# Kernel optimization log

Hardware: AMD Instinct MI355X
Metric: run time of the kernel (lower is better)

The kernel has to match this reference:

```python
import jax, jax.numpy as jnp
import numpy as np

B, S, D = 4, 2048, 512
H = 8
DEPTH = D // H  # 64


def setup_inputs() -> dict:
    key = jax.random.key(0)
    ks = jax.random.split(key, 6)
    scale = 1.0 / np.sqrt(D)
    return {
        "x": jax.random.normal(ks[0], (B, S, D), dtype=jnp.float32),
        "y": jax.random.normal(ks[1], (B, S, D), dtype=jnp.float32),
        "W_q": jax.random.normal(ks[2], (D, D), dtype=jnp.float32) * scale,
        "W_k": jax.random.normal(ks[3], (D, D), dtype=jnp.float32) * scale,
        "W_v": jax.random.normal(ks[4], (D, D), dtype=jnp.float32) * scale,
        "W_o": jax.random.normal(ks[5], (D, D), dtype=jnp.float32) * scale,
    }


def _split_heads(t):
    # [B, S, D] -> [B, H, S, DEPTH]
    b, s, _ = t.shape
    return t.reshape(b, s, H, DEPTH).transpose(0, 2, 1, 3)


def reference(x, y, W_q, W_k, W_v, W_o):
    q = _split_heads(x @ W_q) * (DEPTH ** -0.5)   # [B,H,Sq,d]
    k = _split_heads(y @ W_k)                      # [B,H,Sk,d]
    v = _split_heads(y @ W_v)                      # [B,H,Sk,d]
    logits = jnp.einsum("bhqd,bhkd->bhqk", q, k)   # [B,H,Sq,Sk]
    weights = jax.nn.softmax(logits, axis=-1)
    attn = jnp.einsum("bhqk,bhkd->bhqd", weights, v)  # [B,H,Sq,d]
    attn = attn.transpose(0, 2, 1, 3).reshape(x.shape[0], x.shape[1], D)
    return attn @ W_o
```

## Files before the change

kernel.cpp:

```cpp
#include <hip/hip_runtime.h>
#include <hip/hip_bf16.h>
#include <math.h>
#include <stdint.h>

#define NB 4
#define NS 2048
#define ND 512
#define NH 8
#define DEP 64

typedef __attribute__((ext_vector_type(8))) short bf16x8;
typedef __attribute__((ext_vector_type(4))) short bf16x4;
typedef __attribute__((ext_vector_type(4))) float f32x4;

#define QSCALE 0.18033688011112042f

__device__ __forceinline__ short f2b(float f) {
  unsigned u = __float_as_uint(f);
  u += 0x7FFF + ((u >> 16) & 1);
  return (short)(u >> 16);
}
__device__ __forceinline__ unsigned pk2(float a, float b) {
  union { __hip_bfloat162 h; unsigned u; } c;
  c.h = __float22bfloat162_rn(float2{a, b});
  return c.u;
}
__device__ __forceinline__ void dma16(const void* g, void* l) {
  __builtin_amdgcn_global_load_lds(
      (const __attribute__((address_space(1))) void*)g,
      (__attribute__((address_space(3))) void*)l, 16, 0, 0);
}

__global__ __launch_bounds__(256) void prep(
    const float* __restrict__ x, const float* __restrict__ y,
    const float* __restrict__ W0, const float* __restrict__ W1,
    const float* __restrict__ W2, const float* __restrict__ W3,
    short* __restrict__ xb, short* __restrict__ yb, short* __restrict__ T0,
    short* __restrict__ T1, short* __restrict__ T2, short* __restrict__ T3) {
  const int t = threadIdx.x;
  if (blockIdx.y < 2) {
    const float* src = blockIdx.y ? y : x;
    short* dst = blockIdx.y ? yb : xb;
    size_t i = ((size_t)blockIdx.x * 256 + t) * 4;
    float4 v = *(const float4*)(src + i);
    bf16x4 o;
    o[0] = f2b(v.x); o[1] = f2b(v.y); o[2] = f2b(v.z); o[3] = f2b(v.w);
    *(bf16x4*)(dst + i) = o;
    return;
  }
  const int bx = blockIdx.x;
  if (bx >= 256) return;
  const int wj = bx >> 6, rem = bx & 63;
  const float* W = wj == 0 ? W0 : wj == 1 ? W1 : wj == 2 ? W2 : W3;
  short* T = wj == 0 ? T0 : wj == 1 ? T1 : wj == 2 ? T2 : T3;
  __shared__ float tile[64][65];
  const int k0 = (rem >> 3) * 64, n0 = (rem & 7) * 64;
#pragma unroll
  for (int i = 0; i < 4; ++i) {
    int r = (t >> 4) + i * 16;
    int c = (t & 15) * 4;
    float4 v = *(const float4*)&W[(size_t)(k0 + r) * ND + n0 + c];
    tile[r][c] = v.x; tile[r][c + 1] = v.y;
    tile[r][c + 2] = v.z; tile[r][c + 3] = v.w;
  }
  __syncthreads();
#pragma unroll
  for (int i = 0; i < 4; ++i) {
    int n = (t >> 4) + i * 16;
    int kc = (t & 15) * 4;
    bf16x4 o;
#pragma unroll
    for (int j = 0; j < 4; ++j) o[j] = f2b(tile[kc + j][n]);
    *(bf16x4*)&T[(size_t)(n0 + n) * ND + k0 + kc] = o;
  }
}

__device__ __forceinline__ void gemm128(const short* __restrict__ A,
                                        const short* __restrict__ Bt,
                                        short* __restrict__ Cout, int mode,
                                        float alpha) {
  __shared__ short As[128 * 64];
  __shared__ short Bs[128 * 64];
  const int t = threadIdx.x;
  const int wave = t >> 6, lane = t & 63;
  const int m = lane & 15, quad = lane >> 4;
  const int m0 = blockIdx.y * 128, n0 = blockIdx.x * 128;
  const int mh = (wave >> 1) * 64, nh = (wave & 1) * 64;
  const int r8 = lane >> 3;
  const int c8 = (lane & 7) ^ r8;
  const int mx7 = m & 7;
  f32x4 acc[4][4];
#pragma unroll
  for (int i = 0; i < 4; ++i)
#pragma unroll
    for (int j = 0; j < 4; ++j) acc[i][j] = (f32x4){0.f, 0.f, 0.f, 0.f};

  for (int k0 = 0; k0 < ND; k0 += 64) {
    __syncthreads();
#pragma unroll
    for (int i = 0; i < 4; ++i) {
      int row = i * 32 + wave * 8 + r8;
      dma16(A + (size_t)(m0 + row) * ND + k0 + c8 * 8,
            As + (i * 256 + wave * 64) * 8);
      dma16(Bt + (size_t)(n0 + row) * ND + k0 + c8 * 8,
            Bs + (i * 256 + wave * 64) * 8);
    }
    __syncthreads();
    bf16x8 af[4][2], bf[4][2];
#pragma unroll
    for (int mt = 0; mt < 4; ++mt)
#pragma unroll
      for (int kc = 0; kc < 2; ++kc)
        af[mt][kc] = *(const bf16x8*)(As + (mh + mt * 16 + m) * 64 +
                                      ((kc * 4 + quad) ^ mx7) * 8);
#pragma unroll
    for (int nt = 0; nt < 4; ++nt)
#pragma unroll
      for (int kc = 0; kc < 2; ++kc)
        bf[nt][kc] = *(const bf16x8*)(Bs + (nh + nt * 16 + m) * 64 +
                                      ((kc * 4 + quad) ^ mx7) * 8);
#pragma unroll
    for (int mt = 0; mt < 4; ++mt)
#pragma unroll
      for (int nt = 0; nt < 4; ++nt)
#pragma unroll
        for (int kc = 0; kc < 2; ++kc)
          acc[mt][nt] = __builtin_amdgcn_mfma_f32_16x16x32_bf16(
              af[mt][kc], bf[nt][kc], acc[mt][nt], 0, 0, 0);
  }
  if (mode == 2) {
#pragma unroll
    for (int mt = 0; mt < 4; ++mt)
#pragma unroll
      for (int nt = 0; nt < 4; ++nt) {
        int row0 = m0 + mh + mt * 16 + quad * 4;
        int col = n0 + nh + nt * 16 + m;
        int b_ = row0 >> 11, s_ = row0 & (NS - 1);
        int h_ = col >> 6, d_ = col & (DEP - 1);
        uint2 p;
        p.x = pk2(acc[mt][nt][0] * alpha, acc[mt][nt][1] * alpha);
        p.y = pk2(acc[mt][nt][2] * alpha, acc[mt][nt][3] * alpha);
        *(uint2*)(Cout + (size_t)((b_ * NH + h_) * DEP + d_) * NS + s_) = p;
      }
  } else {
#pragma unroll
    for (int mt = 0; mt < 4; ++mt)
#pragma unroll
      for (int nt = 0; nt < 4; ++nt)
#pragma unroll
        for (int r = 0; r < 4; ++r) {
          int row = m0 + mh + mt * 16 + quad * 4 + r;
          int col = n0 + nh + nt * 16 + m;
          Cout[(size_t)row * ND + col] = f2b(acc[mt][nt][r] * alpha);
        }
  }
}

__global__ __launch_bounds__(256) void qkv_gemm(
    const short* __restrict__ xb, const short* __restrict__ yb,
    const short* __restrict__ Wqt, const short* __restrict__ Wkt,
    const short* __restrict__ Wvt, short* __restrict__ Qb,
    short* __restrict__ Kb, short* __restrict__ Vtb) {
  if (blockIdx.z == 0)
    gemm128(xb, Wqt, Qb, 1, QSCALE);
  else if (blockIdx.z == 1)
    gemm128(yb, Wkt, Kb, 1, 1.0f);
  else
    gemm128(yb, Wvt, Vtb, 2, 1.0f);
}

__global__ __launch_bounds__(256) void out_gemm(const short* __restrict__ A,
                                                const short* __restrict__ Bt,
                                                float* __restrict__ Cout) {
  __shared__ short As[2][128 * 64];
  __shared__ short Bs[2][64 * 64];
  const int t = threadIdx.x;
  const int wave = t >> 6, lane = t & 63;
  const int m = lane & 15, quad = lane >> 4;
  const int m0 = blockIdx.y * 128, n0 = blockIdx.x * 64;
  const int mh = (wave >> 1) * 64, nh = (wave & 1) * 32;
  const int r8 = lane >> 3;
  const int c8 = (lane & 7) ^ r8;
  const int mx7 = m & 7;
  f32x4 acc[4][2];
#pragma unroll
  for (int i = 0; i < 4; ++i)
#pragma unroll
    for (int j = 0; j < 2; ++j) acc[i][j] = (f32x4){0.f, 0.f, 0.f, 0.f};

#pragma unroll
  for (int i = 0; i < 4; ++i)
    dma16(A + (size_t)(m0 + i * 32 + wave * 8 + r8) * ND + c8 * 8,
          As[0] + (i * 256 + wave * 64) * 8);
#pragma unroll
  for (int i = 0; i < 2; ++i)
    dma16(Bt + (size_t)(n0 + i * 32 + wave * 8 + r8) * ND + c8 * 8,
          Bs[0] + (i * 256 + wave * 64) * 8);

  int buf = 0;
  for (int k0 = 0; k0 < ND; k0 += 64, buf ^= 1) {
    __syncthreads();
    if (k0 + 64 < ND) {
#pragma unroll
      for (int i = 0; i < 4; ++i)
        dma16(A + (size_t)(m0 + i * 32 + wave * 8 + r8) * ND + k0 + 64 + c8 * 8,
              As[buf ^ 1] + (i * 256 + wave * 64) * 8);
#pragma unroll
      for (int i = 0; i < 2; ++i)
        dma16(Bt + (size_t)(n0 + i * 32 + wave * 8 + r8) * ND + k0 + 64 +
                  c8 * 8,
              Bs[buf ^ 1] + (i * 256 + wave * 64) * 8);
    }
    bf16x8 af[4][2], bf[2][2];
#pragma unroll
    for (int mt = 0; mt < 4; ++mt)
#pragma unroll
      for (int kc = 0; kc < 2; ++kc)
        af[mt][kc] = *(const bf16x8*)(As[buf] + (mh + mt * 16 + m) * 64 +
                                      ((kc * 4 + quad) ^ mx7) * 8);
#pragma unroll
    for (int nt = 0; nt < 2; ++nt)
#pragma unroll
      for (int kc = 0; kc < 2; ++kc)
        bf[nt][kc] = *(const bf16x8*)(Bs[buf] + (nh + nt * 16 + m) * 64 +
                                      ((kc * 4 + quad) ^ mx7) * 8);
#pragma unroll
    for (int mt = 0; mt < 4; ++mt)
#pragma unroll
      for (int nt = 0; nt < 2; ++nt)
#pragma unroll
        for (int kc = 0; kc < 2; ++kc)
          acc[mt][nt] = __builtin_amdgcn_mfma_f32_16x16x32_bf16(
              af[mt][kc], bf[nt][kc], acc[mt][nt], 0, 0, 0);
  }
#pragma unroll
  for (int mt = 0; mt < 4; ++mt)
#pragma unroll
    for (int nt = 0; nt < 2; ++nt)
#pragma unroll
      for (int r = 0; r < 4; ++r) {
        int row = m0 + mh + mt * 16 + quad * 4 + r;
        int col = n0 + nh + nt * 16 + m;
        Cout[(size_t)row * ND + col] = acc[mt][nt][r];
      }
}

__global__ __launch_bounds__(256) void attn_mfma(const short* __restrict__ Qb,
                                                 const short* __restrict__ Kb,
                                                 const short* __restrict__ Vtb,
                                                 short* __restrict__ Ob) {
  __shared__ short Ks[2][64 * 64];
  __shared__ short Vts[2][64 * 64];
  __shared__ short Pt[64 * 64];
  const int t = threadIdx.x;
  const int wave = t >> 6, lane = t & 63;
  const int m = lane & 15, quad = lane >> 4;
  const int bh = blockIdx.y, b = bh >> 3, h = bh & 7;
  const int q0 = blockIdx.x * 64;
  const int wq = wave * 16;
  const size_t rowb = (size_t)b * NS;
  const short* Vtbase = Vtb + (size_t)(bh * DEP) * NS;
  const int r8 = lane >> 3;
  const int c8 = (lane & 7) ^ r8;
  const int mx7 = m & 7;

  bf16x8 qf[2];
#pragma unroll
  for (int kc = 0; kc < 2; ++kc)
    qf[kc] = *(const bf16x8*)(Qb + (rowb + q0 + wq + m) * ND + h * DEP +
                              kc * 32 + quad * 8);

  float l_ = 0.0f;
  f32x4 Ot[4];
#pragma unroll
  for (int mt = 0; mt < 4; ++mt) Ot[mt] = (f32x4){0.f, 0.f, 0.f, 0.f};

#pragma unroll
  for (int i = 0; i < 2; ++i) {
    int row = i * 32 + wave * 8 + r8;
    dma16(Kb + (rowb + row) * ND + h * DEP + c8 * 8,
          Ks[0] + (i * 256 + wave * 64) * 8);
    dma16(Vtbase + (size_t)row * NS + c8 * 8,
          Vts[0] + (i * 256 + wave * 64) * 8);
  }

  int buf = 0;
  for (int kv0 = 0; kv0 < NS; kv0 += 64, buf ^= 1) {
    __syncthreads();
    if (kv0 + 64 < NS) {
#pragma unroll
      for (int i = 0; i < 2; ++i) {
        int row = i * 32 + wave * 8 + r8;
        dma16(Kb + (rowb + kv0 + 64 + row) * ND + h * DEP + c8 * 8,
              Ks[buf ^ 1] + (i * 256 + wave * 64) * 8);
        dma16(Vtbase + (size_t)row * NS + kv0 + 64 + c8 * 8,
              Vts[buf ^ 1] + (i * 256 + wave * 64) * 8);
      }
    }

    f32x4 St[4];
#pragma unroll
    for (int mt = 0; mt < 4; ++mt) St[mt] = (f32x4){0.f, 0.f, 0.f, 0.f};
#pragma unroll
    for (int mt = 0; mt < 4; ++mt)
#pragma unroll
      for (int kc = 0; kc < 2; ++kc) {
        bf16x8 kf = *(const bf16x8*)(Ks[buf] + (mt * 16 + m) * 64 +
                                     ((kc * 4 + quad) ^ mx7) * 8);
        St[mt] = __builtin_amdgcn_mfma_f32_16x16x32_bf16(kf, qf[kc], St[mt],
                                                         0, 0, 0);
      }

    float rs = 0.0f;
#pragma unroll
    for (int mt = 0; mt < 4; ++mt) {
      float p0 = __builtin_amdgcn_exp2f(St[mt][0]);
      float p1 = __builtin_amdgcn_exp2f(St[mt][1]);
      float p2 = __builtin_amdgcn_exp2f(St[mt][2]);
      float p3 = __builtin_amdgcn_exp2f(St[mt][3]);
      rs += (p0 + p1) + (p2 + p3);
      uint2 pk;
      pk.x = pk2(p0, p1);
      pk.y = pk2(p2, p3);
      *(uint2*)(Pt + (wq + m) * 64 + ((mt * 2 + (quad >> 1)) ^ mx7) * 8 +
                (quad & 1) * 4) = pk;
    }
    l_ += rs;

#pragma unroll
    for (int kc = 0; kc < 2; ++kc) {
      bf16x8 pf = *(const bf16x8*)(Pt + (wq + m) * 64 +
                                   ((kc * 4 + quad) ^ mx7) * 8);
#pragma unroll
      for (int mt = 0; mt < 4; ++mt) {
        bf16x8 vf = *(const bf16x8*)(Vts[buf] + (mt * 16 + m) * 64 +
                                     ((kc * 4 + quad) ^ mx7) * 8);
        Ot[mt] = __builtin_amdgcn_mfma_f32_16x16x32_bf16(vf, pf, Ot[mt],
                                                         0, 0, 0);
      }
    }
  }

  l_ += __shfl_xor(l_, 16, 64);
  l_ += __shfl_xor(l_, 32, 64);
  float linv = 1.0f / l_;
  size_t row = rowb + q0 + wq + m;
#pragma unroll
  for (int mt = 0; mt < 4; ++mt)
#pragma unroll
    for (int r = 0; r < 4; ++r)
      Ob[row * ND + h * DEP + mt * 16 + quad * 4 + r] = f2b(Ot[mt][r] * linv);
}

extern "C" void kernel_launch(void* const* d_in, const int* in_sizes, int n_in,
                              void* d_out, int out_size, void* d_ws,
                              size_t ws_size, hipStream_t stream) {
  const float* x = (const float*)d_in[0];
  const float* y = (const float*)d_in[1];
  const float* Wq = (const float*)d_in[2];
  const float* Wk = (const float*)d_in[3];
  const float* Wv = (const float*)d_in[4];
  const float* Wo = (const float*)d_in[5];
  float* out = (float*)d_out;

  const size_t mat = (size_t)NB * NS * ND;
  const size_t wsz = (size_t)ND * ND;
  short* xb = (short*)d_ws;
  short* yb = xb + mat;
  short* Wqt = yb + mat;
  short* Wkt = Wqt + wsz;
  short* Wvt = Wkt + wsz;
  short* Wot = Wvt + wsz;
  short* Qb = Wot + wsz;
  short* Kb = Qb + mat;
  short* Vtb = Kb + mat;
  short* attnb = xb;

  prep<<<dim3(mat / 1024, 3), 256, 0, stream>>>(x, y, Wq, Wk, Wv, Wo, xb, yb,
                                                Wqt, Wkt, Wvt, Wot);
  qkv_gemm<<<dim3(ND / 128, (NB * NS) / 128, 3), 256, 0, stream>>>(
      xb, yb, Wqt, Wkt, Wvt, Qb, Kb, Vtb);
  attn_mfma<<<dim3(NS / 64, NB * NH), 256, 0, stream>>>(Qb, Kb, Vtb, attnb);
  out_gemm<<<dim3(ND / 64, (NB * NS) / 128), 256, 0, stream>>>(attnb, Wot,
                                                               out);
}
```

Baseline: 186.4 us.

## Fuse K/V projections sharing y tiles and split attention KV across waves

The QKV GEMM now uses 128x64 tiles. The z=1 blocks compute both K and V from one shared y tile, so y is loaded once for both projections, though Q and KV blocks now carry uneven work. The attention kernel changes its wave split: each wave handles 32 queries against half of each 64-key tile instead of 16 queries against the whole tile. Partial outputs and row sums are then combined through shared memory at the end, which adds an epilogue sync and reduction in exchange for better reuse of K fragments.

```diff
diff --git a/kernel.cpp b/kernel.cpp
--- a/kernel.cpp
+++ b/kernel.cpp
@@ -75,38 +75,52 @@
   }
 }
 
-__device__ __forceinline__ void gemm128(const short* __restrict__ A,
-                                        const short* __restrict__ Bt,
-                                        short* __restrict__ Cout, int mode,
-                                        float alpha) {
+__global__ __launch_bounds__(256) void qkv_gemm(
+    const short* __restrict__ xb, const short* __restrict__ yb,
+    const short* __restrict__ Wqt, const short* __restrict__ Wkt,
+    const short* __restrict__ Wvt, short* __restrict__ Qb,
+    short* __restrict__ Kb, short* __restrict__ Vtb) {
   __shared__ short As[128 * 64];
-  __shared__ short Bs[128 * 64];
+  __shared__ short B0s[64 * 64];
+  __shared__ short B1s[64 * 64];
+  const int z = blockIdx.z;
+  const short* A = z ? yb : xb;
+  const short* Bt0 = z ? Wkt : Wqt;
   const int t = threadIdx.x;
   const int wave = t >> 6, lane = t & 63;
   const int m = lane & 15, quad = lane >> 4;
-  const int m0 = blockIdx.y * 128, n0 = blockIdx.x * 128;
-  const int mh = (wave >> 1) * 64, nh = (wave & 1) * 64;
+  const int m0 = blockIdx.y * 128, n0 = blockIdx.x * 64;
+  const int mh = (wave >> 1) * 64, nh = (wave & 1) * 32;
   const int r8 = lane >> 3;
   const int c8 = (lane & 7) ^ r8;
   const int mx7 = m & 7;
-  f32x4 acc[4][4];
+  f32x4 acc0[4][2], acc1[4][2];
 #pragma unroll
   for (int i = 0; i < 4; ++i)
 #pragma unroll
-    for (int j = 0; j < 4; ++j) acc[i][j] = (f32x4){0.f, 0.f, 0.f, 0.f};
+    for (int j = 0; j < 2; ++j) {
+      acc0[i][j] = (f32x4){0.f, 0.f, 0.f, 0.f};
+      acc1[i][j] = (f32x4){0.f, 0.f, 0.f, 0.f};
+    }
 
   for (int k0 = 0; k0 < ND; k0 += 64) {
     __syncthreads();
 #pragma unroll
-    for (int i = 0; i < 4; ++i) {
-      int row = i * 32 + wave * 8 + r8;
-      dma16(A + (size_t)(m0 + row) * ND + k0 + c8 * 8,
+    for (int i = 0; i < 4; ++i)
+      dma16(A + (size_t)(m0 + i * 32 + wave * 8 + r8) * ND + k0 + c8 * 8,
             As + (i * 256 + wave * 64) * 8);
-      dma16(Bt + (size_t)(n0 + row) * ND + k0 + c8 * 8,
-            Bs + (i * 256 + wave * 64) * 8);
+#pragma unroll
+    for (int i = 0; i < 2; ++i)
+      dma16(Bt0 + (size_t)(n0 + i * 32 + wave * 8 + r8) * ND + k0 + c8 * 8,
+            B0s + (i * 256 + wave * 64) * 8);
+    if (z) {
+#pragma unroll
+      for (int i = 0; i < 2; ++i)
+        dma16(Wvt + (size_t)(n0 + i * 32 + wave * 8 + r8) * ND + k0 + c8 * 8,
+              B1s + (i * 256 + wave * 64) * 8);
     }
     __syncthreads();
-    bf16x8 af[4][2], bf[4][2];
+    bf16x8 af[4][2], bf0[2][2];
 #pragma unroll
     for (int mt = 0; mt < 4; ++mt)
 #pragma unroll
@@ -114,59 +128,64 @@
         af[mt][kc] = *(const bf16x8*)(As + (mh + mt * 16 + m) * 64 +
                                       ((kc * 4 + quad) ^ mx7) * 8);
 #pragma unroll
-    for (int nt = 0; nt < 4; ++nt)
+    for (int nt = 0; nt < 2; ++nt)
 #pragma unroll
       for (int kc = 0; kc < 2; ++kc)
-        bf[nt][kc] = *(const bf16x8*)(Bs + (nh + nt * 16 + m) * 64 +
-                                      ((kc * 4 + quad) ^ mx7) * 8);
-#pragma unroll
-    for (int mt = 0; mt < 4; ++mt)
-#pragma unroll
-      for (int nt = 0; nt < 4; ++nt)
+        bf0[nt][kc] = *(const bf16x8*)(B0s + (nh + nt * 16 + m) * 64 +
+                                       ((kc * 4 + quad) ^ mx7) * 8);
+#pragma unroll
+    for (int mt = 0; mt < 4; ++mt)
+#pragma unroll
+      for (int nt = 0; nt < 2; ++nt)
 #pragma unroll
         for (int kc = 0; kc < 2; ++kc)
-          acc[mt][nt] = __builtin_amdgcn_mfma_f32_16x16x32_bf16(
-              af[mt][kc], bf[nt][kc], acc[mt][nt], 0, 0, 0);
-  }
-  if (mode == 2) {
-#pragma unroll
-    for (int mt = 0; mt < 4; ++mt)
-#pragma unroll
-      for (int nt = 0; nt < 4; ++nt) {
+          acc0[mt][nt] = __builtin_amdgcn_mfma_f32_16x16x32_bf16(
+              af[mt][kc], bf0[nt][kc], acc0[mt][nt], 0, 0, 0);
+    if (z) {
+      bf16x8 bf1[2][2];
+#pragma unroll
+      for (int nt = 0; nt < 2; ++nt)
+#pragma unroll
+        for (int kc = 0; kc < 2; ++kc)
+          bf1[nt][kc] = *(const bf16x8*)(B1s + (nh + nt * 16 + m) * 64 +
+                                         ((kc * 4 + quad) ^ mx7) * 8);
+#pragma unroll
+      for (int mt = 0; mt < 4; ++mt)
+#pragma unroll
+        for (int nt = 0; nt < 2; ++nt)
+#pragma unroll
+          for (int kc = 0; kc < 2; ++kc)
+            acc1[mt][nt] = __builtin_amdgcn_mfma_f32_16x16x32_bf16(
+                af[mt][kc], bf1[nt][kc], acc1[mt][nt], 0, 0, 0);
+    }
+  }
+  short* C0 = z ? Kb : Qb;
+  const float alpha0 = z ? 1.0f : QSCALE;
+#pragma unroll
+  for (int mt = 0; mt < 4; ++mt)
+#pragma unroll
+    for (int nt = 0; nt < 2; ++nt)
+#pragma unroll
+      for (int r = 0; r < 4; ++r) {
+        int row = m0 + mh + mt * 16 + quad * 4 + r;
+        int col = n0 + nh + nt * 16 + m;
+        C0[(size_t)row * ND + col] = f2b(acc0[mt][nt][r] * alpha0);
+      }
+  if (z) {
+#pragma unroll
+    for (int mt = 0; mt < 4; ++mt)
+#pragma unroll
+      for (int nt = 0; nt < 2; ++nt) {
         int row0 = m0 + mh + mt * 16 + quad * 4;
         int col = n0 + nh + nt * 16 + m;
         int b_ = row0 >> 11, s_ = row0 & (NS - 1);
         int h_ = col >> 6, d_ = col & (DEP - 1);
         uint2 p;
-        p.x = pk2(acc[mt][nt][0] * alpha, acc[mt][nt][1] * alpha);
-        p.y = pk2(acc[mt][nt][2] * alpha, acc[mt][nt][3] * alpha);
-        *(uint2*)(Cout + (size_t)((b_ * NH + h_) * DEP + d_) * NS + s_) = p;
-      }
-  } else {
-#pragma unroll
-    for (int mt = 0; mt < 4; ++mt)
-#pragma unroll
-      for (int nt = 0; nt < 4; ++nt)
-#pragma unroll
-        for (int r = 0; r < 4; ++r) {
-          int row = m0 + mh + mt * 16 + quad * 4 + r;
-          int col = n0 + nh + nt * 16 + m;
-          Cout[(size_t)row * ND + col] = f2b(acc[mt][nt][r] * alpha);
-        }
-  }
-}
-
-__global__ __launch_bounds__(256) void qkv_gemm(
-    const short* __restrict__ xb, const short* __restrict__ yb,
-    const short* __restrict__ Wqt, const short* __restrict__ Wkt,
-    const short* __restrict__ Wvt, short* __restrict__ Qb,
-    short* __restrict__ Kb, short* __restrict__ Vtb) {
-  if (blockIdx.z == 0)
-    gemm128(xb, Wqt, Qb, 1, QSCALE);
-  else if (blockIdx.z == 1)
-    gemm128(yb, Wkt, Kb, 1, 1.0f);
-  else
-    gemm128(yb, Wvt, Vtb, 2, 1.0f);
+        p.x = pk2(acc1[mt][nt][0], acc1[mt][nt][1]);
+        p.y = pk2(acc1[mt][nt][2], acc1[mt][nt][3]);
+        *(uint2*)(Vtb + (size_t)((b_ * NH + h_) * DEP + d_) * NS + s_) = p;
+      }
+  }
 }
 
 __global__ __launch_bounds__(256) void out_gemm(const short* __restrict__ A,
@@ -255,25 +274,30 @@
   const int t = threadIdx.x;
   const int wave = t >> 6, lane = t & 63;
   const int m = lane & 15, quad = lane >> 4;
+  const int kh = wave >> 1, qh = wave & 1;
   const int bh = blockIdx.y, b = bh >> 3, h = bh & 7;
   const int q0 = blockIdx.x * 64;
-  const int wq = wave * 16;
   const size_t rowb = (size_t)b * NS;
   const short* Vtbase = Vtb + (size_t)(bh * DEP) * NS;
   const int r8 = lane >> 3;
   const int c8 = (lane & 7) ^ r8;
   const int mx7 = m & 7;
 
-  bf16x8 qf[2];
-#pragma unroll
-  for (int kc = 0; kc < 2; ++kc)
-    qf[kc] = *(const bf16x8*)(Qb + (rowb + q0 + wq + m) * ND + h * DEP +
-                              kc * 32 + quad * 8);
-
-  float l_ = 0.0f;
-  f32x4 Ot[4];
-#pragma unroll
-  for (int mt = 0; mt < 4; ++mt) Ot[mt] = (f32x4){0.f, 0.f, 0.f, 0.f};
+  bf16x8 qf[2][2];
+#pragma unroll
+  for (int nt = 0; nt < 2; ++nt)
+#pragma unroll
+    for (int kc = 0; kc < 2; ++kc)
+      qf[nt][kc] =
+          *(const bf16x8*)(Qb + (rowb + q0 + qh * 32 + nt * 16 + m) * ND +
+                           h * DEP + kc * 32 + quad * 8);
+
+  float l_[2] = {0.0f, 0.0f};
+  f32x4 Ot[4][2];
+#pragma unroll
+  for (int mt = 0; mt < 4; ++mt)
+#pragma unroll
+    for (int nt = 0; nt < 2; ++nt) Ot[mt][nt] = (f32x4){0.f, 0.f, 0.f, 0.f};
 
 #pragma unroll
   for (int i = 0; i < 2; ++i) {
@@ -298,58 +322,101 @@
       }
     }
 
-    f32x4 St[4];
-#pragma unroll
-    for (int mt = 0; mt < 4; ++mt) St[mt] = (f32x4){0.f, 0.f, 0.f, 0.f};
-#pragma unroll
-    for (int mt = 0; mt < 4; ++mt)
+    f32x4 St[2][2];
+#pragma unroll
+    for (int mt = 0; mt < 2; ++mt)
+#pragma unroll
+      for (int nt = 0; nt < 2; ++nt) St[mt][nt] = (f32x4){0.f, 0.f, 0.f, 0.f};
+#pragma unroll
+    for (int mt = 0; mt < 2; ++mt)
 #pragma unroll
       for (int kc = 0; kc < 2; ++kc) {
-        bf16x8 kf = *(const bf16x8*)(Ks[buf] + (mt * 16 + m) * 64 +
-                                     ((kc * 4 + quad) ^ mx7) * 8);
-        St[mt] = __builtin_amdgcn_mfma_f32_16x16x32_bf16(kf, qf[kc], St[mt],
-                                                         0, 0, 0);
-      }
-
-    float rs = 0.0f;
-#pragma unroll
-    for (int mt = 0; mt < 4; ++mt) {
-      float p0 = __builtin_amdgcn_exp2f(St[mt][0]);
-      float p1 = __builtin_amdgcn_exp2f(St[mt][1]);
-      float p2 = __builtin_amdgcn_exp2f(St[mt][2]);
-      float p3 = __builtin_amdgcn_exp2f(St[mt][3]);
-      rs += (p0 + p1) + (p2 + p3);
-      uint2 pk;
-      pk.x = pk2(p0, p1);
-      pk.y = pk2(p2, p3);
-      *(uint2*)(Pt + (wq + m) * 64 + ((mt * 2 + (quad >> 1)) ^ mx7) * 8 +
-                (quad & 1) * 4) = pk;
-    }
-    l_ += rs;
-
-#pragma unroll
-    for (int kc = 0; kc < 2; ++kc) {
-      bf16x8 pf = *(const bf16x8*)(Pt + (wq + m) * 64 +
-                                   ((kc * 4 + quad) ^ mx7) * 8);
+        bf16x8 kf =
+            *(const bf16x8*)(Ks[buf] + (kh * 32 + mt * 16 + m) * 64 +
+                             ((kc * 4 + quad) ^ mx7) * 8);
+#pragma unroll
+        for (int nt = 0; nt < 2; ++nt)
+          St[mt][nt] = __builtin_amdgcn_mfma_f32_16x16x32_bf16(
+              kf, qf[nt][kc], St[mt][nt], 0, 0, 0);
+      }
+
+#pragma unroll
+    for (int nt = 0; nt < 2; ++nt) {
+      float rs = 0.0f;
+#pragma unroll
+      for (int mt = 0; mt < 2; ++mt) {
+        float p0 = __builtin_amdgcn_exp2f(St[mt][nt][0]);
+        float p1 = __builtin_amdgcn_exp2f(St[mt][nt][1]);
+        float p2 = __builtin_amdgcn_exp2f(St[mt][nt][2]);
+        float p3 = __builtin_amdgcn_exp2f(St[mt][nt][3]);
+        rs += (p0 + p1) + (p2 + p3);
+        uint2 pk;
+        pk.x = pk2(p0, p1);
+        pk.y = pk2(p2, p3);
+        *(uint2*)(Pt + (qh * 32 + nt * 16 + m) * 64 +
+                  ((kh * 4 + mt * 2 + (quad >> 1)) ^ mx7) * 8 +
+                  (quad & 1) * 4) = pk;
+      }
+      l_[nt] += rs;
+    }
+
+#pragma unroll
+    for (int nt = 0; nt < 2; ++nt) {
+      bf16x8 pf = *(const bf16x8*)(Pt + (qh * 32 + nt * 16 + m) * 64 +
+                                   ((kh * 4 + quad) ^ mx7) * 8);
 #pragma unroll
       for (int mt = 0; mt < 4; ++mt) {
         bf16x8 vf = *(const bf16x8*)(Vts[buf] + (mt * 16 + m) * 64 +
-                                     ((kc * 4 + quad) ^ mx7) * 8);
-        Ot[mt] = __builtin_amdgcn_mfma_f32_16x16x32_bf16(vf, pf, Ot[mt],
-                                                         0, 0, 0);
-      }
-    }
-  }
-
-  l_ += __shfl_xor(l_, 16, 64);
-  l_ += __shfl_xor(l_, 32, 64);
-  float linv = 1.0f / l_;
-  size_t row = rowb + q0 + wq + m;
-#pragma unroll
-  for (int mt = 0; mt < 4; ++mt)
-#pragma unroll
-    for (int r = 0; r < 4; ++r)
-      Ob[row * ND + h * DEP + mt * 16 + quad * 4 + r] = f2b(Ot[mt][r] * linv);
+                                     ((kh * 4 + quad) ^ mx7) * 8);
+        Ot[mt][nt] = __builtin_amdgcn_mfma_f32_16x16x32_bf16(vf, pf, Ot[mt][nt],
+                                                             0, 0, 0);
+      }
+    }
+  }
+
+#pragma unroll
+  for (int nt = 0; nt < 2; ++nt) {
+    l_[nt] += __shfl_xor(l_[nt], 16, 64);
+    l_[nt] += __shfl_xor(l_[nt], 32, 64);
+  }
+  float* obuf = (float*)Ks;
+  float* lv = (float*)Vts;
+  if (kh == 1) {
+    float* dst = obuf + (qh * 64 + lane) * 32;
+#pragma unroll
+    for (int mt = 0; mt < 4; ++mt)
+#pragma unroll
+      for (int nt = 0; nt < 2; ++nt)
+#pragma unroll
+        for (int r = 0; r < 4; ++r) dst[mt * 8 + nt * 4 + r] = Ot[mt][nt][r];
+    if (quad == 0) {
+      lv[qh * 32 + m] = l_[0];
+      lv[qh * 32 + 16 + m] = l_[1];
+    }
+  }
+  __syncthreads();
+  if (kh == 0) {
+    const float* src = obuf + (qh * 64 + lane) * 32;
+    float linv[2];
+#pragma unroll
+    for (int nt = 0; nt < 2; ++nt)
+      linv[nt] = 1.0f / (l_[nt] + lv[qh * 32 + nt * 16 + m]);
+#pragma unroll
+    for (int nt = 0; nt < 2; ++nt) {
+      size_t row = rowb + q0 + qh * 32 + nt * 16 + m;
+#pragma unroll
+      for (int mt = 0; mt < 4; ++mt) {
+        float v0 = (Ot[mt][nt][0] + src[mt * 8 + nt * 4 + 0]) * linv[nt];
+        float v1 = (Ot[mt][nt][1] + src[mt * 8 + nt * 4 + 1]) * linv[nt];
+        float v2 = (Ot[mt][nt][2] + src[mt * 8 + nt * 4 + 2]) * linv[nt];
+        float v3 = (Ot[mt][nt][3] + src[mt * 8 + nt * 4 + 3]) * linv[nt];
+        uint2 p;
+        p.x = pk2(v0, v1);
+        p.y = pk2(v2, v3);
+        *(uint2*)(Ob + row * ND + h * DEP + mt * 16 + quad * 4) = p;
+      }
+    }
+  }
 }
 
 extern "C" void kernel_launch(void* const* d_in, const int* in_sizes, int n_in,
@@ -378,7 +445,7 @@
 
   prep<<<dim3(mat / 1024, 3), 256, 0, stream>>>(x, y, Wq, Wk, Wv, Wo, xb, yb,
                                                 Wqt, Wkt, Wvt, Wot);
-  qkv_gemm<<<dim3(ND / 128, (NB * NS) / 128, 3), 256, 0, stream>>>(
+  qkv_gemm<<<dim3(ND / 64, (NB * NS) / 128, 2), 256, 0, stream>>>(
       xb, yb, Wqt, Wkt, Wvt, Qb, Kb, Vtb);
   attn_mfma<<<dim3(NS / 64, NB * NH), 256, 0, stream>>>(Qb, Kb, Vtb, attnb);
   out_gemm<<<dim3(ND / 64, (NB * NS) / 128), 256, 0, stream>>>(attnb, Wot,
```

After: 201.1 us. 1.08x slower.
